# Kernel tuning notes

Hardware: AMD Instinct MI355X
Metric: run time of the kernel (lower is better)

Reference implementation:

```python
import jax, jax.numpy as jnp
import numpy as np

D_MODEL = 512
DQ = D_MODEL // 4  # 128
TIME_SHIFT_START = 256
VELOCITY_START = 768
NOTE_OFF_START = 128


def conv1d(x, w, b, stride, pad):
    # x: [B, Cin, L], w: [Cout, Cin, K]
    y = jax.lax.conv_general_dilated(x, w, (stride,), [(pad, pad)],
                                     dimension_numbers=('NCH', 'OIH', 'NCH'))
    return y + b[None, :, None]


def adaptive_avg_pool1d(x, out_size):
    # faithful to torch AdaptiveAvgPool1d bin boundaries
    L = x.shape[-1]
    starts = (np.arange(out_size) * L) // out_size
    ends = np.ceil((np.arange(out_size) + 1) * L / out_size).astype(np.int64)
    cs = jnp.concatenate([jnp.zeros(x.shape[:-1] + (1,), x.dtype),
                          jnp.cumsum(x, axis=-1)], axis=-1)
    return (cs[..., ends] - cs[..., starts]) / jnp.asarray(ends - starts, x.dtype)


def setup_inputs() -> dict:
    key = jax.random.key(0)
    ks = jax.random.split(key, 20)

    def w(k, shape):
        fan_in = int(np.prod(shape[1:]))
        return jax.random.normal(k, shape, jnp.float32) / np.sqrt(fan_in)

    def b(k, n):
        return jax.random.normal(k, (n,), jnp.float32) * 0.01

    return {
        'tokens': jax.random.randint(ks[0], (32, 4096), 0, 774),
        'r1_w': w(ks[1], (32, 1, 8)),    'r1_b': b(ks[2], 32),
        'r2_w': w(ks[3], (64, 32, 4)),   'r2_b': b(ks[4], 64),
        'h1_w': w(ks[5], (64, 128, 12)), 'h1_b': b(ks[6], 64),
        'h2_w': w(ks[7], (32, 64, 8)),   'h2_b': b(ks[8], 32),
        'm1_w': w(ks[9], (64, 128, 5)),  'm1_b': b(ks[10], 64),
        'm2_w': w(ks[11], (32, 64, 3)),  'm2_b': b(ks[12], 32),
        'd1_w': w(ks[13], (16, 6, 4)),   'd1_b': b(ks[14], 16),
        'd2_w': w(ks[15], (16, 16, 3)),  'd2_b': b(ks[16], 16),
        'fc_w': w(ks[17], (D_MODEL, D_MODEL)), 'fc_b': b(ks[18], D_MODEL),
    }


def reference(tokens, r1_w, r1_b, r2_w, r2_b, h1_w, h1_b, h2_w, h2_b,
              m1_w, m1_b, m2_w, m2_b, d1_w, d1_b, d2_w, d2_b, fc_w, fc_b):
    B, S = tokens.shape
    relu = jax.nn.relu

    # rhythm: binary time-shift indicator [B,1,S]
    ts = ((tokens >= TIME_SHIFT_START) & (tokens < VELOCITY_START)).astype(jnp.float32)[:, None, :]
    r = relu(conv1d(ts, r1_w, r1_b, 2, 3))
    r = relu(conv1d(r, r2_w, r2_b, 2, 1))
    r = adaptive_avg_pool1d(r, DQ).reshape(B, -1)  # [B, 64*DQ]

    # vectorized one-hot pitch scatter (replaces the python double loop): [B,128,S]
    nm = tokens < NOTE_OFF_START
    pitch = jnp.transpose(
        jax.nn.one_hot(jnp.where(nm, tokens, 0) % 128, 128, dtype=jnp.float32)
        * nm[..., None].astype(jnp.float32), (0, 2, 1))

    h = relu(conv1d(pitch, h1_w, h1_b, 1, 6))
    h = relu(conv1d(h, h2_w, h2_b, 2, 3))
    h = adaptive_avg_pool1d(h, DQ).reshape(B, -1)  # [B, 32*DQ]

    m = relu(conv1d(pitch, m1_w, m1_b, 1, 2))
    m = relu(conv1d(m, m2_w, m2_b, 1, 1))
    m = adaptive_avg_pool1d(m, DQ).reshape(B, -1)  # [B, 32*DQ]

    # velocity one-hot scatter: [B,6,S]
    vm = tokens >= VELOCITY_START
    vel = jnp.clip(jnp.where(vm, tokens - VELOCITY_START, 0), 0, 5)
    vpat = jnp.transpose(
        jax.nn.one_hot(vel, 6, dtype=jnp.float32) * vm[..., None].astype(jnp.float32),
        (0, 2, 1))
    d = relu(conv1d(vpat, d1_w, d1_b, 1, 2))
    d = relu(conv1d(d, d2_w, d2_b, 1, 1))
    d = adaptive_avg_pool1d(d, DQ).reshape(B, -1)  # [B, 16*DQ]

    # total flattened size is 36*d_model != d_model, so torch branch always pools
    r, h, m, d = [adaptive_avg_pool1d(f[:, None, :], DQ)[:, 0] for f in (r, h, m, d)]

    combined = jnp.concatenate([r, h, m, d], axis=1)       # [B, d_model]
    feats = combined @ fc_w.T + fc_b                        # Linear
    return jnp.broadcast_to(feats[:, None, :], (B, S, D_MODEL))
```

## Files before the change

### kernel.cpp

```cpp
#include <hip/hip_runtime.h>

typedef unsigned short u16;
typedef unsigned int u32;
typedef float vf4 __attribute__((ext_vector_type(4)));
typedef unsigned int vu4 __attribute__((ext_vector_type(4)));
typedef short sh8 __attribute__((ext_vector_type(8)));
typedef float f32x4 __attribute__((ext_vector_type(4)));

__device__ __forceinline__ float bf2f(u16 u) {
  return __uint_as_float(((u32)u) << 16);
}
__device__ __forceinline__ u16 f2bf(float f) {
  u32 x = __float_as_uint(f);
  return (u16)((x + 0x7fffu + ((x >> 16) & 1u)) >> 16);
}
__device__ __forceinline__ float ldin(const void* p, int idx, int isf) {
  return isf ? ((const float*)p)[idx] : bf2f(((const u16*)p)[idx]);
}

#define OFF_FLAG  ((size_t)0)
#define OFF_WB    ((size_t)16)
#define OFF_WTH1  ((size_t)1180432)
#define OFF_WTM1  ((size_t)1573648)
#define OFF_COMB  ((size_t)1737488)
#define OFF_FEATF ((size_t)1803024)
#define OFF_FEATB ((size_t)1868560)
#define OFF_R1    ((size_t)1901328)
#define OFF_D1    ((size_t)10289936)
#define OFF_DP    ((size_t)18686736)
#define OFF_H1    ((size_t)18948880)
#define OFF_M1    ((size_t)35758864)
#define OFF_WH2B  ((size_t)52536080)
#define OFF_WH2L  ((size_t)52568848)
#define OFF_WM2B  ((size_t)52601616)
#define OFF_WM2L  ((size_t)52613904)
#define WS_NEEDED ((size_t)52626192)

#define WB_R1W 0
#define WB_R1B 256
#define WB_R2W 288
#define WB_R2B 8480
#define WB_H1B 8544
#define WB_H2W 8608
#define WB_H2B 24992
#define WB_M1B 25024
#define WB_M2W 25088
#define WB_M2B 31232
#define WB_D1W 31264
#define WB_D1B 31648
#define WB_D2W 31664
#define WB_D2B 32432
#define WB_FCW 32448
#define WB_FCB 294592
#define WB_TOTAL 295104

#define H1_STRIDE 4104
#define D1_STRIDE 4100

__global__ __launch_bounds__(256) void k_detect(const u16* __restrict__ fcw_raw,
                                                int* __restrict__ flagp) {
  __shared__ int cnt[4];
  int tid = threadIdx.x;
  u16 v = fcw_raw[2 * tid];
  int e = (v >> 7) & 0xFF;
  int outside = (e < 100 || e > 140) ? 1 : 0;
  unsigned long long m = __ballot(outside);
  if ((tid & 63) == 0) cnt[tid >> 6] = __popcll(m);
  __syncthreads();
  if (tid == 0) flagp[0] = (cnt[0] + cnt[1] + cnt[2] + cnt[3] >= 64) ? 1 : 0;
}

__global__ __launch_bounds__(256) void k_convert(
    const void* r1_w, const void* r1_b, const void* r2_w, const void* r2_b,
    const void* h1_w, const void* h1_b, const void* h2_w, const void* h2_b,
    const void* m1_w, const void* m1_b, const void* m2_w, const void* m2_b,
    const void* d1_w, const void* d1_b, const void* d2_w, const void* d2_b,
    const void* fc_w, const void* fc_b,
    const int* __restrict__ flagp, float* __restrict__ wb,
    float* __restrict__ wTh1, float* __restrict__ wTm1,
    float* __restrict__ combined,
    u16* __restrict__ wh2b, u16* __restrict__ wh2l,
    u16* __restrict__ wm2b, u16* __restrict__ wm2l) {
  int j = blockIdx.x * 256 + threadIdx.x;
  if (j >= 473280) return;
  int isf = flagp[0];
  if (j < WB_TOTAL) {
    const void* src; int si;
    if      (j < WB_R1B) { src = r1_w; si = j; }
    else if (j < WB_R2W) { src = r1_b; si = j - WB_R1B; }
    else if (j < WB_R2B) { src = r2_w; si = j - WB_R2W; }
    else if (j < WB_H1B) { src = r2_b; si = j - WB_R2B; }
    else if (j < WB_H2W) { src = h1_b; si = j - WB_H1B; }
    else if (j < WB_H2B) { src = h2_w; si = j - WB_H2W; }
    else if (j < WB_M1B) { src = h2_b; si = j - WB_H2B; }
    else if (j < WB_M2W) { src = m1_b; si = j - WB_M1B; }
    else if (j < WB_M2B) { src = m2_w; si = j - WB_M2W; }
    else if (j < WB_D1W) { src = m2_b; si = j - WB_M2B; }
    else if (j < WB_D1B) { src = d1_w; si = j - WB_D1W; }
    else if (j < WB_D2W) { src = d1_b; si = j - WB_D1B; }
    else if (j < WB_D2B) { src = d2_w; si = j - WB_D2W; }
    else if (j < WB_FCW) { src = d2_b; si = j - WB_D2B; }
    else if (j < WB_FCB) { src = fc_w; si = j - WB_FCW; }
    else                 { src = fc_b; si = j - WB_FCB; }
    wb[j] = ldin(src, si, isf);
  } else if (j < 393408) {
    int j2 = j - WB_TOTAL;
    int o = j2 & 63, r = j2 >> 6, k = r % 12, p = r / 12;
    wTh1[j2] = ldin(h1_w, (o * 128 + p) * 12 + k, isf);
  } else if (j < 434368) {
    int j3 = j - 393408;
    int o = j3 & 63, r = j3 >> 6, k = r % 5, p = r / 5;
    wTm1[j3] = ldin(m1_w, (o * 128 + p) * 5 + k, isf);
  } else if (j < 450752) {
    combined[j - 434368] = 0.f;
  } else if (j < 467136) {
    int jj = j - 450752;
    int o = jj >> 9, rem = jj & 511, c = rem >> 3, kk = rem & 7;
    float w = ldin(h2_w, (o * 64 + c) * 8 + kk, isf);
    u16 hi = f2bf(w);
    wh2b[jj] = hi;
    wh2l[jj] = f2bf(w - bf2f(hi));
  } else {
    int jj = j - 467136;
    int o = jj / 192, rem = jj % 192, c = rem / 3, kk = rem % 3;
    float w = ldin(m2_w, (o * 64 + c) * 3 + kk, isf);
    u16 hi = f2bf(w);
    wm2b[jj] = hi;
    wm2l[jj] = f2bf(w - bf2f(hi));
  }
}


__device__ __forceinline__ void dev_r1(float* smem, const int* tok,
                                       const float* r1wf, const float* r1bf,
                                       float* r1ws, int chunk, int b) {
  float* w1s = smem;
  float* b1s = smem + 256;
  float* Ibuf = smem + 288;
  int tid = threadIdx.x;
  w1s[tid] = r1wf[tid];
  if (tid < 32) b1s[tid] = r1bf[tid];
  int t0 = chunk * 64;
  if (tid < 134) {
    int x = 2 * t0 - 3 + tid;
    float v = 0.f;
    if ((unsigned)x < 4096u) {
      int tk = tok[b * 4096 + x];
      v = (tk >= 256 && tk < 768) ? 1.f : 0.f;
    }
    Ibuf[tid] = v;
  }
  __syncthreads();
  int tl = tid & 63, og = tid >> 6;
  float iv[8];
#pragma unroll
  for (int k = 0; k < 8; ++k) iv[k] = Ibuf[2 * tl + k];
  int t = t0 + tl;
#pragma unroll
  for (int i = 0; i < 8; ++i) {
    int o = og * 8 + i;
    float acc = b1s[o];
#pragma unroll
    for (int k = 0; k < 8; ++k) acc = fmaf(w1s[o * 8 + k], iv[k], acc);
    r1ws[(size_t)(b * 32 + o) * 2048 + t] = fmaxf(acc, 0.f);
  }
}

__device__ __forceinline__ void dev_d1(float* smem, const int* tok,
                                       const float* d1wf, const float* d1bf,
                                       float* d1ws, int chunk, int b) {
  float* wds = smem;
  int* cls = (int*)(smem + 384);
  int tid = threadIdx.x;
  for (int f = tid; f < 384; f += 256) wds[f] = d1wf[f];
  int t0 = chunk * 64;
  if (tid < 67) {
    int x = t0 - 2 + tid;
    int v = -1;
    if ((unsigned)x < 4096u) {
      int tk = tok[b * 4096 + x];
      if (tk >= 768) { v = tk - 768; v = v > 5 ? 5 : v; }
    }
    cls[tid] = v;
  }
  __syncthreads();
  int tl = tid & 63, og = tid >> 6;
  int t = t0 + tl;
  if (t > 4096) return;
  int vk[4];
#pragma unroll
  for (int k = 0; k < 4; ++k) vk[k] = cls[tl + k];
#pragma unroll
  for (int i = 0; i < 4; ++i) {
    int o = og * 4 + i;
    float acc = d1bf[o];
#pragma unroll
    for (int k = 0; k < 4; ++k) {
      int v = vk[k];
      if (v >= 0) acc += wds[(o * 6 + v) * 4 + k];
    }
    d1ws[(size_t)(b * 16 + o) * D1_STRIDE + t] = fmaxf(acc, 0.f);
  }
}

__device__ __forceinline__ void dev_h1(float* smem, const int* tok,
                                       const float* wTh1, const float* h1bf,
                                       u16* h1ws, int bx, int b) {
  float (*tile)[65] = reinterpret_cast<float(*)[65]>(smem);
  int tid = threadIdx.x;
  int t0 = bx * 32;
  int o = tid & 63, sub = tid >> 6;
  float bias = h1bf[o];
#pragma unroll
  for (int j = 0; j < 8; ++j) {
    int tl = j * 4 + sub;
    int t = t0 + tl;
    float acc = bias;
    if (t <= 4096) {
#pragma unroll
      for (int k = 0; k < 12; ++k) {
        int x = t + k - 6;
        if ((unsigned)x < 4096u) {
          int p = tok[b * 4096 + x];
          if (p < 128) acc += wTh1[(p * 12 + k) * 64 + o];
        }
      }
    }
    tile[tl][o] = fmaxf(acc, 0.f);
  }
  __syncthreads();
  int o2 = tid >> 2, seg = tid & 3;
  size_t rowbase = (size_t)(b * 64 + o2) * H1_STRIDE;
  int ts = t0 + seg * 8;
  if (ts + 7 <= 4096) {
    u32 w0 = (u32)f2bf(tile[seg * 8 + 0][o2]) | ((u32)f2bf(tile[seg * 8 + 1][o2]) << 16);
    u32 w1 = (u32)f2bf(tile[seg * 8 + 2][o2]) | ((u32)f2bf(tile[seg * 8 + 3][o2]) << 16);
    u32 w2 = (u32)f2bf(tile[seg * 8 + 4][o2]) | ((u32)f2bf(tile[seg * 8 + 5][o2]) << 16);
    u32 w3 = (u32)f2bf(tile[seg * 8 + 6][o2]) | ((u32)f2bf(tile[seg * 8 + 7][o2]) << 16);
    uint4 v; v.x = w0; v.y = w1; v.z = w2; v.w = w3;
    *(uint4*)&h1ws[rowbase + ts] = v;
  } else {
    for (int i2 = 0; i2 < 8; ++i2) {
      int t = ts + i2;
      if (t <= 4096) h1ws[rowbase + t] = f2bf(tile[seg * 8 + i2][o2]);
    }
  }
}

__device__ __forceinline__ void dev_m1(float* smem, const int* tok,
                                       const float* wTm1, const float* m1bf,
                                       u16* m1ws, int bx, int b) {
  float (*tile)[65] = reinterpret_cast<float(*)[65]>(smem);
  int tid = threadIdx.x;
  int t0 = bx * 32;
  int o = tid & 63, sub = tid >> 6;
  float bias = m1bf[o];
#pragma unroll
  for (int j = 0; j < 8; ++j) {
    int tl = j * 4 + sub;
    int t = t0 + tl;
    float acc = bias;
#pragma unroll
    for (int k = 0; k < 5; ++k) {
      int x = t + k - 2;
      if ((unsigned)x < 4096u) {
        int p = tok[b * 4096 + x];
        if (p < 128) acc += wTm1[(p * 5 + k) * 64 + o];
      }
    }
    tile[tl][o] = fmaxf(acc, 0.f);
  }
  __syncthreads();
  int o2 = tid >> 2, seg = tid & 3;
  size_t rowbase = (size_t)(b * 64 + o2) * 4096;
  int ts = t0 + seg * 8;
  u32 w0 = (u32)f2bf(tile[seg * 8 + 0][o2]) | ((u32)f2bf(tile[seg * 8 + 1][o2]) << 16);
  u32 w1 = (u32)f2bf(tile[seg * 8 + 2][o2]) | ((u32)f2bf(tile[seg * 8 + 3][o2]) << 16);
  u32 w2 = (u32)f2bf(tile[seg * 8 + 4][o2]) | ((u32)f2bf(tile[seg * 8 + 5][o2]) << 16);
  u32 w3 = (u32)f2bf(tile[seg * 8 + 6][o2]) | ((u32)f2bf(tile[seg * 8 + 7][o2]) << 16);
  uint4 v; v.x = w0; v.y = w1; v.z = w2; v.w = w3;
  *(uint4*)&m1ws[rowbase + ts] = v;
}

__global__ __launch_bounds__(256) void k_cv1(const int* __restrict__ tok,
                                             const float* __restrict__ wb,
                                             const float* __restrict__ wTh1,
                                             const float* __restrict__ wTm1,
                                             float* __restrict__ r1ws,
                                             float* __restrict__ d1ws,
                                             u16* __restrict__ h1ws,
                                             u16* __restrict__ m1ws) {
  __shared__ __align__(16) float smem[2080];
  int bx = blockIdx.x;
  if (bx < 1024) {
    dev_r1(smem, tok, wb + WB_R1W, wb + WB_R1B, r1ws, bx & 31, bx >> 5);
  } else if (bx < 3104) {
    int n = bx - 1024;
    dev_d1(smem, tok, wb + WB_D1W, wb + WB_D1B, d1ws, n % 65, n / 65);
  } else if (bx < 7232) {
    int n = bx - 3104;
    dev_h1(smem, tok, wTh1, wb + WB_H1B, h1ws, n % 129, n / 129);
  } else {
    int n = bx - 7232;
    dev_m1(smem, tok, wTm1, wb + WB_M1B, m1ws, n & 127, n >> 7);
  }
}


__device__ __forceinline__ void dev_h2(float* smem, const u16* h1ws,
                                       const u16* wh2b, const u16* wh2l,
                                       const float* h2bf,
                                       float* combined, int chunk, int q, int b) {
  u16* xs = (u16*)smem;
  const int tid = threadIdx.x;
  const int w = tid >> 6, l = tid & 63;
  const int quad = l >> 4, n = l & 15;
  const int ot = w & 1, tp = w >> 1;
  const int tb = q * 512 + chunk * 64;
  f32x4 acc[2];
  acc[0] = (f32x4){0.f, 0.f, 0.f, 0.f};
  acc[1] = (f32x4){0.f, 0.f, 0.f, 0.f};
  const u16* wph = wh2b + (size_t)(16 * ot + n) * 512 + quad * 8;
  const u16* wpl = wh2l + (size_t)(16 * ot + n) * 512 + quad * 8;

  for (int kc = 0; kc < 2; ++kc) {
    sh8 ah[8], al[8];
#pragma unroll
    for (int s = 0; s < 8; ++s) {
      ah[s] = *(const sh8*)(wph + kc * 256 + 32 * s);
      al[s] = *(const sh8*)(wpl + kc * 256 + 32 * s);
    }
    for (int it = 0; it < 2; ++it) {
      for (int f = tid; f < 1280; f += 256) {
        int rg = f / 640, rem = f % 640, cl = rem / 20, ch = rem % 20;
        int t0 = tb + (2 * it + rg) * 16;
        int xa = 2 * t0 - 4 + 2 * ch;
        const u16* row = h1ws + (size_t)(b * 64 + kc * 32 + cl) * H1_STRIDE;
        u32 vlo = ((unsigned)xa <= 4096u) ? row[xa] : 0u;
        u32 vhi = ((unsigned)(xa + 1) <= 4096u) ? row[xa + 1] : 0u;
        ((u32*)xs)[f] = vlo | (vhi << 16);
      }
      __syncthreads();
      const u16* xr = xs + tp * 1280;
#pragma unroll
      for (int s = 0; s < 8; ++s) {
        const u16* sp = xr + (4 * s + quad) * 40 + 2 * n + 1;
        sh8 bb;
#pragma unroll
        for (int j = 0; j < 8; ++j) bb[j] = (short)sp[j];
        acc[it] = __builtin_amdgcn_mfma_f32_16x16x32_bf16(ah[s], bb, acc[it], 0, 0, 0);
        acc[it] = __builtin_amdgcn_mfma_f32_16x16x32_bf16(al[s], bb, acc[it], 0, 0, 0);
      }
      __syncthreads();
    }
  }
#pragma unroll
  for (int r = 0; r < 4; ++r) {
    float bs = h2bf[16 * ot + quad * 4 + r];
    float s = fmaxf(acc[0][r] + bs, 0.f) + fmaxf(acc[1][r] + bs, 0.f);
    s += __shfl_xor(s, 1, 64);
    s += __shfl_xor(s, 2, 64);
    s += __shfl_xor(s, 4, 64);
    s += __shfl_xor(s, 8, 64);
    if (n == 0) {
      int o = 16 * ot + quad * 4 + r;
      atomicAdd(&combined[b * 512 + 128 + 4 * o + q], s * (1.f / 512.f));
    }
  }
}

__device__ __forceinline__ void dev_m2(float* smem, const u16* m1ws,
                                       const u16* wm2b, const u16* wm2l,
                                       const float* m2bf,
                                       float* combined, int sub, int q, int b) {
  u16* xs = (u16*)smem;
  const int tid = threadIdx.x;
  const int w = tid >> 6, l = tid & 63;
  const int quad = l >> 4, n = l & 15;
  const int ot = w & 1, tp = w >> 1;
  const int tb = q * 1024 + sub * 256;
  sh8 ah[6], al[6];
  {
    const u16* wph = wm2b + (size_t)(16 * ot + n) * 192 + quad * 8;
    const u16* wpl = wm2l + (size_t)(16 * ot + n) * 192 + quad * 8;
#pragma unroll
    for (int s = 0; s < 6; ++s) {
      ah[s] = *(const sh8*)(wph + 32 * s);
      al[s] = *(const sh8*)(wpl + 32 * s);
    }
  }
  float bs[4];
#pragma unroll
  for (int r = 0; r < 4; ++r) bs[r] = m2bf[16 * ot + quad * 4 + r];
  float sm[4] = {0.f, 0.f, 0.f, 0.f};
  const int gkb = quad * 8;

  for (int it = 0; it < 8; ++it) {
    for (int f = tid; f < 1280; f += 256) {
      int rg = f / 640, rem = f % 640, c = rem / 10, ch = rem % 10;
      int t0 = tb + (2 * it + rg) * 16;
      int xa = t0 - 2 + 2 * ch;
      const u16* row = m1ws + (size_t)(b * 64 + c) * 4096;
      u32 vlo = ((unsigned)xa < 4096u) ? row[xa] : 0u;
      u32 vhi = ((unsigned)(xa + 1) < 4096u) ? row[xa + 1] : 0u;
      ((u32*)xs)[f] = vlo | (vhi << 16);
    }
    __syncthreads();
    const u16* xr = xs + tp * 1280;
    f32x4 acc = {0.f, 0.f, 0.f, 0.f};
#pragma unroll
    for (int s = 0; s < 6; ++s) {
      sh8 bb;
#pragma unroll
      for (int j = 0; j < 8; ++j) {
        int gk = 32 * s + gkb + j;
        int c = (gk * 21846) >> 16;
        int kk = gk - 3 * c;
        bb[j] = (short)xr[c * 20 + n + kk + 1];
      }
      acc = __builtin_amdgcn_mfma_f32_16x16x32_bf16(ah[s], bb, acc, 0, 0, 0);
      acc = __builtin_amdgcn_mfma_f32_16x16x32_bf16(al[s], bb, acc, 0, 0, 0);
    }
#pragma unroll
    for (int r = 0; r < 4; ++r) sm[r] += fmaxf(acc[r] + bs[r], 0.f);
    __syncthreads();
  }
#pragma unroll
  for (int r = 0; r < 4; ++r) {
    float s = sm[r];
    s += __shfl_xor(s, 1, 64);
    s += __shfl_xor(s, 2, 64);
    s += __shfl_xor(s, 4, 64);
    s += __shfl_xor(s, 8, 64);
    if (n == 0) {
      int o = 16 * ot + quad * 4 + r;
      atomicAdd(&combined[b * 512 + 256 + 4 * o + q], s * (1.f / 1024.f));
    }
  }
}

__device__ __forceinline__ void dev_r2(float* smem, const float* r1ws,
                                       const float* r2wf, const float* r2bf,
                                       float* combined, int chunk, int b) {
  float* wcr = smem;
  float (*tile)[68] = reinterpret_cast<float(*)[68]>(smem + 2048);
  const int tbase = chunk * 64;
  const int half = chunk >> 3;
  const int tid = threadIdx.x;
  const int og = tid >> 6, tl = tid & 63;
  float acc[16];
#pragma unroll
  for (int i = 0; i < 16; ++i) acc[i] = 0.f;

  for (int c0 = 0; c0 < 32; c0 += 8) {
    for (int f = tid; f < 2048; f += 256) {
      int o = f & 63, r = f >> 6, k = r & 3, cc = r >> 2;
      wcr[f] = r2wf[(o * 32 + c0 + cc) * 4 + k];
    }
    for (int f = tid; f < 1056; f += 256) {
      int iu = f % 66, pc = f / 66, p = pc & 1, cc = pc >> 1;
      int x = 2 * (tbase - 1 + iu) + p;
      float v = 0.f;
      if (x >= 0 && x < 2048) v = r1ws[(size_t)(b * 32 + c0 + cc) * 2048 + x];
      tile[pc][iu] = v;
    }
    __syncthreads();
#pragma unroll
    for (int cc = 0; cc < 8; ++cc) {
      float ev[3], od[3];
#pragma unroll
      for (int f3 = 0; f3 < 3; ++f3) {
        ev[f3] = tile[cc * 2][tl + f3];
        od[f3] = tile[cc * 2 + 1][tl + f3];
      }
#pragma unroll
      for (int k = 0; k < 4; ++k) {
        const int p = (k + 1) & 1, fk = (k + 1) >> 1;
        const float* wv = &wcr[(cc * 4 + k) * 64 + og * 16];
        float4 wa = *(const float4*)wv;
        float4 wbv = *(const float4*)(wv + 4);
        float4 wcc = *(const float4*)(wv + 8);
        float4 wd = *(const float4*)(wv + 12);
        float wr[16] = {wa.x, wa.y, wa.z, wa.w, wbv.x, wbv.y, wbv.z, wbv.w,
                        wcc.x, wcc.y, wcc.z, wcc.w, wd.x, wd.y, wd.z, wd.w};
        float v0 = p ? od[fk] : ev[fk];
#pragma unroll
        for (int i = 0; i < 16; ++i) acc[i] = fmaf(v0, wr[i], acc[i]);
      }
    }
    __syncthreads();
  }
  const float inv = 1.f / 512.f;
#pragma unroll
  for (int i = 0; i < 16; ++i) {
    int o = og * 16 + i;
    float s = fmaxf(acc[i] + r2bf[o], 0.f);
#pragma unroll
    for (int d = 32; d > 0; d >>= 1) s += __shfl_down(s, d, 64);
    if (tl == 0) atomicAdd(&combined[b * 512 + 2 * o + half], s * inv);
  }
}

__device__ __forceinline__ void dev_d2(float* smem, const float* d1ws,
                                       const float* d2wf, const float* d2bf,
                                       float* dpws, int chunk, int b) {
  float* wd = smem;
  float (*dt)[132] = reinterpret_cast<float(*)[132]>(smem + 768);
  float* c2 = smem + 768 + 2112;
  const int tbase = chunk * 128;
  const int tid = threadIdx.x;
  for (int f = tid; f < 768; f += 256) wd[f] = d2wf[f];
  for (int f = tid; f < 2096; f += 256) {
    int iu = f % 131, c = f / 131;
    int x = tbase - 1 + iu;
    float v = 0.f;
    if (x >= 0 && x <= 4096) v = d1ws[(size_t)(b * 16 + c) * D1_STRIDE + x];
    dt[c][iu] = v;
  }
  __syncthreads();
  for (int idx = tid; idx < 16 * 129; idx += 256) {
    int o = idx / 129, tl = idx % 129;
    float acc = d2bf[o];
    const float* w = &wd[o * 48];
#pragma unroll 4
    for (int c = 0; c < 16; ++c) {
      acc = fmaf(dt[c][tl], w[c * 3 + 0],
            fmaf(dt[c][tl + 1], w[c * 3 + 1],
            fmaf(dt[c][tl + 2], w[c * 3 + 2], acc)));
    }
    c2[o * 133 + tl] = fmaxf(acc, 0.f);
  }
  __syncthreads();
  if (tid < 64) {
    int o = tid >> 2, qq = tid & 3;
    const float* row = c2 + o * 133 + 32 * qq;
    float s = 0.f;
#pragma unroll
    for (int j = 0; j < 33; ++j) s += row[j];
    dpws[(size_t)(b * 16 + o) * 128 + 4 * chunk + qq] = s * (1.f / 33.f);
  }
}

__global__ __launch_bounds__(256, 4) void k_cv2(const u16* __restrict__ h1ws,
                                                const u16* __restrict__ m1ws,
                                                const float* __restrict__ r1ws,
                                                const float* __restrict__ d1ws,
                                                const float* __restrict__ wb,
                                                const u16* __restrict__ wh2b,
                                                const u16* __restrict__ wh2l,
                                                const u16* __restrict__ wm2b,
                                                const u16* __restrict__ wm2l,
                                                float* __restrict__ combined,
                                                float* __restrict__ dpws) {
  __shared__ __align__(16) float smem[5008];
  int bx = blockIdx.x;
  if (bx < 1024) {
    dev_h2(smem, h1ws, wh2b, wh2l, wb + WB_H2B, combined, bx & 7, (bx >> 3) & 3, bx >> 5);
  } else if (bx < 1536) {
    int n = bx - 1024;
    dev_m2(smem, m1ws, wm2b, wm2l, wb + WB_M2B, combined, n & 3, (n >> 2) & 3, n >> 4);
  } else if (bx < 2048) {
    int n = bx - 1536;
    dev_r2(smem, r1ws, wb + WB_R2W, wb + WB_R2B, combined, n & 15, n >> 4);
  } else {
    int n = bx - 2048;
    dev_d2(smem, d1ws, wb + WB_D2W, wb + WB_D2B, dpws, n & 31, n >> 5);
  }
}

__global__ __launch_bounds__(256) void k_fc(const float* __restrict__ combined,
                                            const float* __restrict__ dpws,
                                            const float* __restrict__ fcwf,
                                            const float* __restrict__ fcbf,
                                            float* __restrict__ featf,
                                            u16* __restrict__ featb) {
  const int b = blockIdx.x, tid = threadIdx.x;
  __shared__ float cb[512];
  cb[tid] = combined[b * 512 + tid];
  if (tid < 128) {
    cb[256 + tid] = combined[b * 512 + 256 + tid];
  } else {
    int j = tid - 128;
    int o = j >> 3, i0 = (j & 7) * 16;
    const float* row = dpws + (size_t)(b * 16 + o) * 128;
    float s = 0.f;
#pragma unroll
    for (int i = 0; i < 16; ++i) s += row[i0 + i];
    cb[384 + j] = s * (1.f / 16.f);
  }
  __syncthreads();
  for (int h = 0; h < 2; ++h) {
    int oo = h * 256 + tid;
    float acc = fcbf[oo];
    const float4* wr = (const float4*)(fcwf + (size_t)oo * 512);
#pragma unroll 8
    for (int j4 = 0; j4 < 128; ++j4) {
      float4 w = wr[j4];
      const float* c4 = &cb[j4 * 4];
      acc = fmaf(c4[0], w.x, acc);
      acc = fmaf(c4[1], w.y, acc);
      acc = fmaf(c4[2], w.z, acc);
      acc = fmaf(c4[3], w.w, acc);
    }
    featf[b * 512 + oo] = acc;
    featb[b * 512 + oo] = f2bf(acc);
  }
}

__global__ __launch_bounds__(256) void k_bcast(const int* __restrict__ flagp,
                                               const vf4* __restrict__ featf4,
                                               const vu4* __restrict__ featb4,
                                               vf4* __restrict__ outf,
                                               vu4* __restrict__ outb) {
  int base = blockIdx.x * 1024 + threadIdx.x;
  if (flagp[0]) {
#pragma unroll
    for (int s = 0; s < 4; ++s) {
      int g = base + s * 256;
      vf4 v = featf4[(g >> 19) * 128 + (g & 127)];
      __builtin_nontemporal_store(v, &outf[g]);
    }
  } else {
#pragma unroll
    for (int s = 0; s < 4; ++s) {
      int g = base + s * 256;
      if (g < 8388608) {
        vu4 v = featb4[(g >> 18) * 64 + (g & 63)];
        __builtin_nontemporal_store(v, &outb[g]);
      }
    }
  }
}

extern "C" void kernel_launch(void* const* d_in, const int* in_sizes, int n_in,
                              void* d_out, int out_size, void* d_ws, size_t ws_size,
                              hipStream_t stream) {
  if (ws_size < WS_NEEDED) return;

  const int* tokens = (const int*)d_in[0];
  const void* r1_w = d_in[1];  const void* r1_b = d_in[2];
  const void* r2_w = d_in[3];  const void* r2_b = d_in[4];
  const void* h1_w = d_in[5];  const void* h1_b = d_in[6];
  const void* h2_w = d_in[7];  const void* h2_b = d_in[8];
  const void* m1_w = d_in[9];  const void* m1_b = d_in[10];
  const void* m2_w = d_in[11]; const void* m2_b = d_in[12];
  const void* d1_w = d_in[13]; const void* d1_b = d_in[14];
  const void* d2_w = d_in[15]; const void* d2_b = d_in[16];
  const void* fc_w = d_in[17]; const void* fc_b = d_in[18];

  char* ws = (char*)d_ws;
  int*   flagp   = (int*)  (ws + OFF_FLAG);
  float* wb      = (float*)(ws + OFF_WB);
  float* wTh1    = (float*)(ws + OFF_WTH1);
  float* wTm1    = (float*)(ws + OFF_WTM1);
  float* combined= (float*)(ws + OFF_COMB);
  float* featf   = (float*)(ws + OFF_FEATF);
  u16*   featb   = (u16*)  (ws + OFF_FEATB);
  float* r1ws    = (float*)(ws + OFF_R1);
  float* d1ws    = (float*)(ws + OFF_D1);
  float* dpws    = (float*)(ws + OFF_DP);
  u16*   h1ws    = (u16*)  (ws + OFF_H1);
  u16*   m1ws    = (u16*)  (ws + OFF_M1);
  u16*   wh2b    = (u16*)  (ws + OFF_WH2B);
  u16*   wh2l    = (u16*)  (ws + OFF_WH2L);
  u16*   wm2b    = (u16*)  (ws + OFF_WM2B);
  u16*   wm2l    = (u16*)  (ws + OFF_WM2L);

  k_detect<<<1, 256, 0, stream>>>((const u16*)fc_w, flagp);
  k_convert<<<1849, 256, 0, stream>>>(r1_w, r1_b, r2_w, r2_b, h1_w, h1_b, h2_w, h2_b,
                                      m1_w, m1_b, m2_w, m2_b, d1_w, d1_b, d2_w, d2_b,
                                      fc_w, fc_b, flagp, wb, wTh1, wTm1, combined,
                                      wh2b, wh2l, wm2b, wm2l);
  k_cv1<<<11328, 256, 0, stream>>>(tokens, wb, wTh1, wTm1, r1ws, d1ws, h1ws, m1ws);
  k_cv2<<<3072, 256, 0, stream>>>(h1ws, m1ws, r1ws, d1ws, wb, wh2b, wh2l, wm2b, wm2l,
                                  combined, dpws);
  k_fc<<<32, 256, 0, stream>>>(combined, dpws, wb + WB_FCW, wb + WB_FCB, featf, featb);
  k_bcast<<<16384, 256, 0, stream>>>(flagp, (const vf4*)featf, (const vu4*)featb,
                                     (vf4*)d_out, (vu4*)d_out);
}
```

Measured before the change: 486.2 us.

## Fold dtype detection into convert kernel and load h2 inputs directly from global

Removes the separate k_detect launch by having every k_convert block recompute the dtype flag from a sample of fc_w, with block 0 still writing it for later kernels. The h2 convolution stage no longer stages h1 activations through shared memory with syncthreads; each lane reads its 8 bf16 operands straight from global with a 16-byte copy, falling back to a masked path at the left edge. To make that safe, the h1 writer now zero-fills the padding past column 4096 up to the row stride, so reads past the valid end return zeros. This trades shared-memory staging and barriers for possibly unaligned, redundant global/L2 reads.

```diff
diff --git a/kernel.cpp b/kernel.cpp
--- a/kernel.cpp
+++ b/kernel.cpp
@@ -57,33 +57,32 @@
 #define H1_STRIDE 4104
 #define D1_STRIDE 4100
 
-__global__ __launch_bounds__(256) void k_detect(const u16* __restrict__ fcw_raw,
-                                                int* __restrict__ flagp) {
-  __shared__ int cnt[4];
-  int tid = threadIdx.x;
-  u16 v = fcw_raw[2 * tid];
-  int e = (v >> 7) & 0xFF;
-  int outside = (e < 100 || e > 140) ? 1 : 0;
-  unsigned long long m = __ballot(outside);
-  if ((tid & 63) == 0) cnt[tid >> 6] = __popcll(m);
-  __syncthreads();
-  if (tid == 0) flagp[0] = (cnt[0] + cnt[1] + cnt[2] + cnt[3] >= 64) ? 1 : 0;
-}
-
 __global__ __launch_bounds__(256) void k_convert(
     const void* r1_w, const void* r1_b, const void* r2_w, const void* r2_b,
     const void* h1_w, const void* h1_b, const void* h2_w, const void* h2_b,
     const void* m1_w, const void* m1_b, const void* m2_w, const void* m2_b,
     const void* d1_w, const void* d1_b, const void* d2_w, const void* d2_b,
     const void* fc_w, const void* fc_b,
-    const int* __restrict__ flagp, float* __restrict__ wb,
+    int* __restrict__ flagp, float* __restrict__ wb,
     float* __restrict__ wTh1, float* __restrict__ wTm1,
     float* __restrict__ combined,
     u16* __restrict__ wh2b, u16* __restrict__ wh2l,
     u16* __restrict__ wm2b, u16* __restrict__ wm2l) {
-  int j = blockIdx.x * 256 + threadIdx.x;
+  __shared__ int cnt[4];
+  int tid = threadIdx.x;
+  {
+    u16 v = ((const u16*)fc_w)[2 * tid];
+    int e = (v >> 7) & 0xFF;
+    int outside = (e < 100 || e > 140) ? 1 : 0;
+    unsigned long long m = __ballot(outside);
+    if ((tid & 63) == 0) cnt[tid >> 6] = __popcll(m);
+  }
+  __syncthreads();
+  int isf = (cnt[0] + cnt[1] + cnt[2] + cnt[3] >= 64) ? 1 : 0;
+  if (blockIdx.x == 0 && tid == 0) flagp[0] = isf;
+
+  int j = blockIdx.x * 256 + tid;
   if (j >= 473280) return;
-  int isf = flagp[0];
   if (j < WB_TOTAL) {
     const void* src; int si;
     if      (j < WB_R1B) { src = r1_w; si = j; }
@@ -243,6 +242,7 @@
     for (int i2 = 0; i2 < 8; ++i2) {
       int t = ts + i2;
       if (t <= 4096) h1ws[rowbase + t] = f2bf(tile[seg * 8 + i2][o2]);
+      else if (t < H1_STRIDE) h1ws[rowbase + t] = 0;
     }
   }
 }
@@ -307,11 +307,10 @@
 }
 
 
-__device__ __forceinline__ void dev_h2(float* smem, const u16* h1ws,
+__device__ __forceinline__ void dev_h2(const u16* h1ws,
                                        const u16* wh2b, const u16* wh2l,
                                        const float* h2bf,
                                        float* combined, int chunk, int q, int b) {
-  u16* xs = (u16*)smem;
   const int tid = threadIdx.x;
   const int w = tid >> 6, l = tid & 63;
   const int quad = l >> 4, n = l & 15;
@@ -330,28 +329,27 @@
       ah[s] = *(const sh8*)(wph + kc * 256 + 32 * s);
       al[s] = *(const sh8*)(wpl + kc * 256 + 32 * s);
     }
+#pragma unroll
     for (int it = 0; it < 2; ++it) {
-      for (int f = tid; f < 1280; f += 256) {
-        int rg = f / 640, rem = f % 640, cl = rem / 20, ch = rem % 20;
-        int t0 = tb + (2 * it + rg) * 16;
-        int xa = 2 * t0 - 4 + 2 * ch;
-        const u16* row = h1ws + (size_t)(b * 64 + kc * 32 + cl) * H1_STRIDE;
-        u32 vlo = ((unsigned)xa <= 4096u) ? row[xa] : 0u;
-        u32 vhi = ((unsigned)(xa + 1) <= 4096u) ? row[xa + 1] : 0u;
-        ((u32*)xs)[f] = vlo | (vhi << 16);
-      }
-      __syncthreads();
-      const u16* xr = xs + tp * 1280;
+      int t0 = tb + (2 * it + tp) * 16;
+      int xbase = 2 * t0 + 2 * n - 3;
 #pragma unroll
       for (int s = 0; s < 8; ++s) {
-        const u16* sp = xr + (4 * s + quad) * 40 + 2 * n + 1;
+        int c = kc * 32 + 4 * s + quad;
+        const u16* row = h1ws + (size_t)(b * 64 + c) * H1_STRIDE;
         sh8 bb;
-#pragma unroll
-        for (int j = 0; j < 8; ++j) bb[j] = (short)sp[j];
+        if (xbase >= 0) {
+          __builtin_memcpy(&bb, row + xbase, 16);
+        } else {
+#pragma unroll
+          for (int j = 0; j < 8; ++j) {
+            int x = xbase + j;
+            bb[j] = (x >= 0) ? (short)row[x] : (short)0;
+          }
+        }
         acc[it] = __builtin_amdgcn_mfma_f32_16x16x32_bf16(ah[s], bb, acc[it], 0, 0, 0);
         acc[it] = __builtin_amdgcn_mfma_f32_16x16x32_bf16(al[s], bb, acc[it], 0, 0, 0);
       }
-      __syncthreads();
     }
   }
 #pragma unroll
@@ -555,7 +553,7 @@
   __shared__ __align__(16) float smem[5008];
   int bx = blockIdx.x;
   if (bx < 1024) {
-    dev_h2(smem, h1ws, wh2b, wh2l, wb + WB_H2B, combined, bx & 7, (bx >> 3) & 3, bx >> 5);
+    dev_h2(h1ws, wh2b, wh2l, wb + WB_H2B, combined, bx & 7, (bx >> 3) & 3, bx >> 5);
   } else if (bx < 1536) {
     int n = bx - 1024;
     dev_m2(smem, m1ws, wm2b, wm2l, wb + WB_M2B, combined, n & 3, (n >> 2) & 3, n >> 4);
@@ -666,7 +664,6 @@
   u16*   wm2b    = (u16*)  (ws + OFF_WM2B);
   u16*   wm2l    = (u16*)  (ws + OFF_WM2L);
 
-  k_detect<<<1, 256, 0, stream>>>((const u16*)fc_w, flagp);
   k_convert<<<1849, 256, 0, stream>>>(r1_w, r1_b, r2_w, r2_b, h1_w, h1_b, h2_w, h2_b,
                                       m1_w, m1_b, m2_w, m2_b, d1_w, d1_b, d2_w, d2_b,
                                       fc_w, fc_b, flagp, wb, wTh1, wTm1, combined,
```

Measured after the change: 482.8 us, median of 2. About the same (-0.7%).
